# Kernel tuning notes

Measured on AMD Instinct MI355X. Metric: run time of the kernel, lower is better.

## Reference

```python
import jax, jax.numpy as jnp
import numpy as np

D_MODEL = 1024
N_HEADS = 16
HEAD_DIM = D_MODEL // N_HEADS
BATCH = 1
SEQLEN = 4096


def setup_inputs() -> dict:
    key = jax.random.key(0)
    k1, k2, k3 = jax.random.split(key, 3)
    x = jax.random.normal(k1, (BATCH, SEQLEN, D_MODEL), dtype=jnp.float32)
    # match typical Dense init scale so softmax isn't saturated
    Wqkv = jax.random.normal(k2, (D_MODEL, 3 * D_MODEL), dtype=jnp.float32) / np.sqrt(D_MODEL)
    Wout = jax.random.normal(k3, (D_MODEL, D_MODEL), dtype=jnp.float32) / np.sqrt(D_MODEL)
    return {"x": x, "Wqkv": Wqkv, "Wout": Wout}


def reference(x, Wqkv, Wout):
    b, l, d = x.shape
    qkv = x @ Wqkv  # [b, l, 3d]
    q, k, v = jnp.split(qkv, 3, axis=-1)
    # [b, l, d] -> [b, h, l, hd]
    def to_heads(t):
        return t.reshape(b, l, N_HEADS, HEAD_DIM).transpose(0, 2, 1, 3)
    q, k, v = to_heads(q), to_heads(k), to_heads(v)
    scale = 1.0 / np.sqrt(HEAD_DIM)
    attn = jnp.einsum('bhld,bhsd->bhls', q, k) * scale  # [b,h,l,l]
    causal_mask = jnp.tril(jnp.ones((l, l), dtype=bool))
    attn = jnp.where(causal_mask, attn, -jnp.inf)
    attn = jax.nn.softmax(attn, axis=-1)
    out = jnp.einsum('bhls,bhsd->bhld', attn, v)  # [b,h,l,hd]
    out = out.transpose(0, 2, 1, 3).reshape(b, l, d)
    return out @ Wout
```

## Files before the change

### kernel.cpp

```cpp
#include <hip/hip_runtime.h>

#define SEQ 4096
#define DM 1024
#define NH 16
#define HD 64

typedef __attribute__((ext_vector_type(8))) short short8;
typedef __attribute__((ext_vector_type(4))) short short4v;
typedef __attribute__((ext_vector_type(2))) short short2v;
typedef __attribute__((ext_vector_type(4))) float float4v;
typedef __attribute__((ext_vector_type(4))) int int4v;

__device__ __forceinline__ short f2bf(float f) {
    union { float f; unsigned u; } v; v.f = f;
    unsigned u = v.u;
    return (short)((u + 0x7fffu + ((u >> 16) & 1u)) >> 16);
}
__device__ __forceinline__ int cvtpk(float lo, float hi) {
    int r;
    asm("v_cvt_pk_bf16_f32 %0, %1, %2" : "=v"(r) : "v"(lo), "v"(hi));
    return r;
}

__device__ __forceinline__ void gload_lds16(const void* g, void* l) {
    __builtin_amdgcn_global_load_lds(
        (const __attribute__((address_space(1))) void*)g,
        (__attribute__((address_space(3))) void*)l, 16, 0, 0);
}

__global__ void cast_x(const float* __restrict__ in, short* __restrict__ out, int n4) {
    int i = blockIdx.x * blockDim.x + threadIdx.x;
    if (i < n4) {
        float4v x = ((const float4v*)in)[i];
        short4v o;
        o[0] = f2bf(x[0]); o[1] = f2bf(x[1]); o[2] = f2bf(x[2]); o[3] = f2bf(x[3]);
        ((short4v*)out)[i] = o;
    }
}

__global__ void transpose_cast(const float* __restrict__ in, short* __restrict__ out,
                               int H, int W, int scaled_rows, float scale) {
    __shared__ float tile[32][33];
    int bx = blockIdx.x * 32, by = blockIdx.y * 32;
    int tx = threadIdx.x, ty = threadIdx.y;
#pragma unroll
    for (int i = 0; i < 32; i += 8)
        tile[ty + i][tx] = in[(by + ty + i) * W + bx + tx];
    __syncthreads();
#pragma unroll
    for (int i = 0; i < 32; i += 8) {
        int orow = bx + ty + i;
        float sc = (orow < scaled_rows) ? scale : 1.0f;
        out[orow * H + by + tx] = f2bf(tile[tx][ty + i] * sc);
    }
}

__global__ void transpose_v(const short* __restrict__ qkv, short* __restrict__ vt) {
    __shared__ short tile[64][66];
    int h = blockIdx.z;
    int l0 = blockIdx.x * 64;
    int tx = threadIdx.x, ty = threadIdx.y;
#pragma unroll
    for (int i = 0; i < 8; i++) {
        int r = ty + i * 8;
        short2v v = *(const short2v*)&qkv[(l0 + r) * (3 * DM) + 2 * DM + h * HD + 2 * tx];
        tile[r][2 * tx] = v[0];
        tile[r][2 * tx + 1] = v[1];
    }
    __syncthreads();
#pragma unroll
    for (int i = 0; i < 8; i++) {
        int d = ty + i * 8;
        short2v v;
        v[0] = tile[2 * tx][d];
        v[1] = tile[2 * tx + 1][d];
        int s = l0 + 2 * tx;
        int soff = (s & ~31) | ((s & 12) << 1) | ((s & 16) >> 2) | (s & 3);
        *(short2v*)&vt[(h * HD + d) * SEQ + soff] = v;
    }
}

template <typename OutT>
__global__ __launch_bounds__(256) void gemm_bt(const short* __restrict__ A,
                                               const short* __restrict__ BT,
                                               OutT* __restrict__ C,
                                               int M, int N, int K) {
    __shared__ short As[128 * 32];
    __shared__ short Bs[128 * 32];
    int tid  = threadIdx.x;
    int m0   = blockIdx.y * 128;
    int n0   = blockIdx.x * 128;
    int w    = tid >> 6, lane = tid & 63;
    int wm   = w >> 1,  wn   = w & 1;
    int quad = lane >> 4, l15 = lane & 15;
    int srow = lane >> 2;
    int scol = (lane & 3) * 8;

    float4v acc[4][4];
#pragma unroll
    for (int mi = 0; mi < 4; mi++)
#pragma unroll
        for (int ni = 0; ni < 4; ni++)
            acc[mi][ni] = {0.f, 0.f, 0.f, 0.f};

    for (int k0 = 0; k0 < K; k0 += 32) {
        __syncthreads();
#pragma unroll
        for (int t = 0; t < 2; t++) {
            int chunk = w * 2 + t;
            int r = chunk * 16 + srow;
            gload_lds16(&A[(m0 + r) * K + k0 + scol], &As[chunk * 16 * 32]);
            gload_lds16(&BT[(n0 + r) * K + k0 + scol], &Bs[chunk * 16 * 32]);
        }
        __syncthreads();
        short8 a[4], b[4];
#pragma unroll
        for (int mi = 0; mi < 4; mi++)
            a[mi] = *(const short8*)&As[(wm * 64 + mi * 16 + l15) * 32 + quad * 8];
#pragma unroll
        for (int ni = 0; ni < 4; ni++)
            b[ni] = *(const short8*)&Bs[(wn * 64 + ni * 16 + l15) * 32 + quad * 8];
#pragma unroll
        for (int mi = 0; mi < 4; mi++)
#pragma unroll
            for (int ni = 0; ni < 4; ni++)
                acc[mi][ni] = __builtin_amdgcn_mfma_f32_16x16x32_bf16(a[mi], b[ni], acc[mi][ni], 0, 0, 0);
    }

#pragma unroll
    for (int mi = 0; mi < 4; mi++)
#pragma unroll
        for (int ni = 0; ni < 4; ni++)
#pragma unroll
            for (int r = 0; r < 4; r++) {
                int row = m0 + wm * 64 + mi * 16 + quad * 4 + r;
                int col = n0 + wn * 64 + ni * 16 + l15;
                float v = acc[mi][ni][r];
                if constexpr (sizeof(OutT) == 2) C[row * N + col] = (OutT)f2bf(v);
                else                             C[row * N + col] = (OutT)v;
            }
}

__global__ __launch_bounds__(256) void gemm_bt64(const short* __restrict__ A,
                                                 const short* __restrict__ BT,
                                                 float* __restrict__ C,
                                                 int M, int N, int K) {
    __shared__ short As[64 * 32];
    __shared__ short Bs[128 * 32];
    int tid  = threadIdx.x;
    int m0   = blockIdx.y * 64;
    int n0   = blockIdx.x * 128;
    int w    = tid >> 6, lane = tid & 63;
    int wm   = w >> 1,  wn   = w & 1;
    int quad = lane >> 4, l15 = lane & 15;
    int srow = lane >> 2;
    int scol = (lane & 3) * 8;

    float4v acc[2][4];
#pragma unroll
    for (int mi = 0; mi < 2; mi++)
#pragma unroll
        for (int ni = 0; ni < 4; ni++)
            acc[mi][ni] = {0.f, 0.f, 0.f, 0.f};

    for (int k0 = 0; k0 < K; k0 += 32) {
        __syncthreads();
        {
            int r = w * 16 + srow;
            gload_lds16(&A[(m0 + r) * K + k0 + scol], &As[w * 16 * 32]);
        }
#pragma unroll
        for (int t = 0; t < 2; t++) {
            int chunk = w * 2 + t;
            int r = chunk * 16 + srow;
            gload_lds16(&BT[(n0 + r) * K + k0 + scol], &Bs[chunk * 16 * 32]);
        }
        __syncthreads();
        short8 a[2], b[4];
#pragma unroll
        for (int mi = 0; mi < 2; mi++)
            a[mi] = *(const short8*)&As[(wm * 32 + mi * 16 + l15) * 32 + quad * 8];
#pragma unroll
        for (int ni = 0; ni < 4; ni++)
            b[ni] = *(const short8*)&Bs[(wn * 64 + ni * 16 + l15) * 32 + quad * 8];
#pragma unroll
        for (int mi = 0; mi < 2; mi++)
#pragma unroll
            for (int ni = 0; ni < 4; ni++)
                acc[mi][ni] = __builtin_amdgcn_mfma_f32_16x16x32_bf16(a[mi], b[ni], acc[mi][ni], 0, 0, 0);
    }

#pragma unroll
    for (int mi = 0; mi < 2; mi++)
#pragma unroll
        for (int ni = 0; ni < 4; ni++)
#pragma unroll
            for (int r = 0; r < 4; r++) {
                int row = m0 + wm * 32 + mi * 16 + quad * 4 + r;
                int col = n0 + wn * 64 + ni * 16 + l15;
                C[row * N + col] = acc[mi][ni][r];
            }
}

__global__ __launch_bounds__(256, 2) void attn_kernel(const short* __restrict__ qkv,
                                                      const short* __restrict__ vtp,
                                                      float* __restrict__ Of0,
                                                      float* __restrict__ Of1,
                                                      float* __restrict__ Of2,
                                                      float* __restrict__ Lf0,
                                                      float* __restrict__ Lf1,
                                                      float* __restrict__ Lf2) {
    __shared__ short Ks[3][64 * 64];
    __shared__ short Vs[3][64 * 64];
    int gid = blockIdx.x;
    int rr = gid & 7, qq = gid >> 3;
    int hb = qq / 48;
    int rem = qq - hb * 48;
    int h = rr + 8 * hb;
    int b = rem & 15;
    int j = rem >> 4;
    float* __restrict__ Of = (j == 0) ? Of0 : (j == 1) ? Of1 : Of2;
    float* __restrict__ Lf = (j == 0) ? Lf0 : (j == 1) ? Lf1 : Lf2;
    int B0 = 2 * b + 2;

    int tid = threadIdx.x;
    int w = tid >> 6, lane = tid & 63;
    int quad = lane >> 4, l15 = lane & 15;
    int rowb = w * 16;
    int lrow = lane >> 3;
    int cg   = (lane & 7) ^ lrow;
    int xr   = (l15 & 7) * 8;

    const short* Kg = qkv + DM + h * HD;
    const short* Vg = vtp + (h * HD) * SEQ;

    short8 onesv;
#pragma unroll
    for (int i = 0; i < 8; i++) onesv[i] = (short)0x3F80;

#pragma unroll 1
    for (int sg = 0; sg < 2; sg++) {
        int t, st0, stN;
        if (sg == 0) {
            t = b;
            st0 = 22 * j;
            stN = (22 * j + 22 < B0) ? 22 * j + 22 : B0;
        } else {
            t = 31 - b;
            int a0 = 22 * j - B0;
            st0 = (a0 > 0) ? a0 : 0;
            stN = 22 * j + 22 - B0;
        }
        if (st0 >= stN) continue;

        int q0 = t * 128;
        int qw = q0 + w * 32;

        short8 aq[2][2];
#pragma unroll
        for (int mi = 0; mi < 2; mi++)
#pragma unroll
            for (int kk = 0; kk < 2; kk++)
                aq[mi][kk] = *(const short8*)&qkv[(qw + mi * 16 + l15) * (3 * DM) + h * HD + kk * 32 + quad * 8];

        float4v lacc[2];
        float4v o[2][4];
#pragma unroll
        for (int mi = 0; mi < 2; mi++) {
            lacc[mi] = {0.f, 0.f, 0.f, 0.f};
#pragma unroll
            for (int dt = 0; dt < 4; dt++)
                o[mi][dt] = {0.f, 0.f, 0.f, 0.f};
        }

        auto stage = [&](int slot, int tt_) {
            int s0_ = tt_ * 64;
#pragma unroll
            for (int i = 0; i < 2; i++) {
                int r = rowb + i * 8;
                gload_lds16(&Kg[(s0_ + r + lrow) * (3 * DM) + cg * 8], &Ks[slot][r * 64]);
                gload_lds16(&Vg[(r + lrow) * SEQ + s0_ + cg * 8],      &Vs[slot][r * 64]);
            }
        };

        stage(0, st0);
        bool two = (st0 + 1 < stN);
        if (two) {
            stage(1, st0 + 1);
            asm volatile("s_waitcnt vmcnt(4)" ::: "memory");
        } else {
            asm volatile("s_waitcnt vmcnt(0)" ::: "memory");
        }
        __builtin_amdgcn_s_barrier();
        __builtin_amdgcn_sched_barrier(0);

        int sA = 0, sB = 1, sC = 2;
        for (int tt = st0; tt < stN; tt++) {
            int s0 = tt * 64;
            if (tt + 2 < stN) stage(sC, tt + 2);

            const short* Kb = &Ks[sA][0];
            const short* Vb = &Vs[sA][0];

            short8 kc[8], vc[8];
#pragma unroll
            for (int ni = 0; ni < 4; ni++)
#pragma unroll
                for (int kk = 0; kk < 2; kk++)
                    kc[ni * 2 + kk] = *(const short8*)&Kb[(ni * 16 + l15) * 64 + (((kk * 4 + quad) * 8) ^ xr)];
#pragma unroll
            for (int dt = 0; dt < 4; dt++)
#pragma unroll
                for (int pr = 0; pr < 2; pr++)
                    vc[dt * 2 + pr] = *(const short8*)&Vb[(dt * 16 + l15) * 64 + (((pr * 4 + quad) * 8) ^ xr)];

            float4v s[2][4];
            __builtin_amdgcn_s_setprio(1);
#pragma unroll
            for (int mi = 0; mi < 2; mi++)
#pragma unroll
                for (int ni = 0; ni < 4; ni++) {
                    float4v a = {0.f, 0.f, 0.f, 0.f};
#pragma unroll
                    for (int kk = 0; kk < 2; kk++)
                        a = __builtin_amdgcn_mfma_f32_16x16x32_bf16(kc[ni * 2 + kk], aq[mi][kk], a, 0, 0, 0);
                    s[mi][ni] = a;
                }
            __builtin_amdgcn_s_setprio(0);

            bool diag = (s0 + 63 > qw);
            if (diag) {
#pragma unroll
                for (int mi = 0; mi < 2; mi++) {
                    int qrow = qw + mi * 16 + l15;
#pragma unroll
                    for (int ni = 0; ni < 4; ni++)
#pragma unroll
                        for (int r = 0; r < 4; r++) {
                            float p = __builtin_amdgcn_exp2f(s[mi][ni][r]);
                            int scol = s0 + ni * 16 + quad * 4 + r;
                            s[mi][ni][r] = (scol <= qrow) ? p : 0.f;
                        }
                }
            } else {
#pragma unroll
                for (int mi = 0; mi < 2; mi++)
#pragma unroll
                    for (int ni = 0; ni < 4; ni++)
#pragma unroll
                        for (int r = 0; r < 4; r++)
                            s[mi][ni][r] = __builtin_amdgcn_exp2f(s[mi][ni][r]);
            }
            short8 pa[2][2];
#pragma unroll
            for (int mi = 0; mi < 2; mi++)
#pragma unroll
                for (int pr = 0; pr < 2; pr++) {
                    int4v wpk;
                    wpk[0] = cvtpk(s[mi][2 * pr][0], s[mi][2 * pr][1]);
                    wpk[1] = cvtpk(s[mi][2 * pr][2], s[mi][2 * pr][3]);
                    wpk[2] = cvtpk(s[mi][2 * pr + 1][0], s[mi][2 * pr + 1][1]);
                    wpk[3] = cvtpk(s[mi][2 * pr + 1][2], s[mi][2 * pr + 1][3]);
                    pa[mi][pr] = *(short8*)&wpk;
                }

            __builtin_amdgcn_s_setprio(1);
#pragma unroll
            for (int mi = 0; mi < 2; mi++)
#pragma unroll
                for (int pr = 0; pr < 2; pr++)
                    lacc[mi] = __builtin_amdgcn_mfma_f32_16x16x32_bf16(pa[mi][pr], onesv, lacc[mi], 0, 0, 0);
#pragma unroll
            for (int mi = 0; mi < 2; mi++)
#pragma unroll
                for (int dt = 0; dt < 4; dt++)
#pragma unroll
                    for (int pr = 0; pr < 2; pr++)
                        o[mi][dt] = __builtin_amdgcn_mfma_f32_16x16x32_bf16(pa[mi][pr], vc[dt * 2 + pr], o[mi][dt], 0, 0, 0);
            __builtin_amdgcn_s_setprio(0);

            asm volatile("s_waitcnt lgkmcnt(0)" ::: "memory");
            if (tt + 2 < stN) asm volatile("s_waitcnt vmcnt(4)" ::: "memory");
            else              asm volatile("s_waitcnt vmcnt(0)" ::: "memory");
            __builtin_amdgcn_s_barrier();
            __builtin_amdgcn_sched_barrier(0);
            int tmp = sA; sA = sB; sB = sC; sC = tmp;
        }

#pragma unroll
        for (int mi = 0; mi < 2; mi++)
#pragma unroll
            for (int r = 0; r < 4; r++) {
                int row = qw + mi * 16 + quad * 4 + r;
#pragma unroll
                for (int dt = 0; dt < 4; dt++)
                    Of[row * DM + h * HD + dt * 16 + l15] = o[mi][dt][r];
            }
        if (l15 == 0) {
#pragma unroll
            for (int mi = 0; mi < 2; mi++)
#pragma unroll
                for (int r = 0; r < 4; r++)
                    Lf[h * SEQ + qw + mi * 16 + quad * 4 + r] = lacc[mi][r];
        }
    }
}

__global__ void attn_finalize(const float* __restrict__ Of0, const float* __restrict__ Of1,
                              const float* __restrict__ Of2,
                              const float* __restrict__ Lf0, const float* __restrict__ Lf1,
                              const float* __restrict__ Lf2,
                              short* __restrict__ ao) {
    int i = blockIdx.x * blockDim.x + threadIdx.x;
    int q  = i >> 8;
    int c4 = i & 255;
    int h  = c4 >> 4;
    int t  = q >> 7;
    bool lowq = (t < 16);
    int b = lowq ? t : 31 - t;
    bool use0 = lowq || (b <= 9);
    bool use1 = (!lowq) || (b >= 11);
    bool use2 = !lowq;

    float l = 0.f;
    float4v acc = {0.f, 0.f, 0.f, 0.f};
    if (use0) {
        l += Lf0[h * SEQ + q];
        float4v a = ((const float4v*)Of0)[i];
        acc[0] += a[0]; acc[1] += a[1]; acc[2] += a[2]; acc[3] += a[3];
    }
    if (use1) {
        l += Lf1[h * SEQ + q];
        float4v a = ((const float4v*)Of1)[i];
        acc[0] += a[0]; acc[1] += a[1]; acc[2] += a[2]; acc[3] += a[3];
    }
    if (use2) {
        l += Lf2[h * SEQ + q];
        float4v a = ((const float4v*)Of2)[i];
        acc[0] += a[0]; acc[1] += a[1]; acc[2] += a[2]; acc[3] += a[3];
    }
    float inv = 1.0f / l;
    short4v o;
    o[0] = f2bf(acc[0] * inv);
    o[1] = f2bf(acc[1] * inv);
    o[2] = f2bf(acc[2] * inv);
    o[3] = f2bf(acc[3] * inv);
    ((short4v*)ao)[i] = o;
}

extern "C" void kernel_launch(void* const* d_in, const int* in_sizes, int n_in,
                              void* d_out, int out_size, void* d_ws, size_t ws_size,
                              hipStream_t stream) {
    const float* x    = (const float*)d_in[0];
    const float* Wqkv = (const float*)d_in[1];
    const float* Wout = (const float*)d_in[2];
    float* out = (float*)d_out;

    char* ws = (char*)d_ws;
    short* xb    = (short*)(ws);
    short* wqkvT = (short*)(ws + 8388608);
    float* Of0   = (float*)(ws);
    float* Of1   = (float*)(d_out);
    short* qkv   = (short*)(ws + 16777216);
    short* vt    = (short*)(ws + 41943040);
    short* ao    = (short*)(ws + 50331648);
    float* Of2   = (float*)(ws + 58720256);
    float* Lf0   = (float*)(ws + 75497472);
    float* Lf1   = (float*)(ws + 75759616);
    float* Lf2   = (float*)(ws + 76021760);
    short* woutT = (short*)(ws + 76283904);

    const float SC = 0.18033688011112042f;

    cast_x<<<4096, 256, 0, stream>>>(x, xb, (SEQ * DM) / 4);
    transpose_cast<<<dim3(3 * DM / 32, DM / 32), dim3(32, 8), 0, stream>>>(Wqkv, wqkvT, DM, 3 * DM, DM, SC);
    transpose_cast<<<dim3(DM / 32, DM / 32), dim3(32, 8), 0, stream>>>(Wout, woutT, DM, DM, 0, 1.0f);

    gemm_bt<short><<<dim3(3 * DM / 128, SEQ / 128), 256, 0, stream>>>(xb, wqkvT, qkv, SEQ, 3 * DM, DM);

    transpose_v<<<dim3(SEQ / 64, 1, NH), dim3(32, 8), 0, stream>>>(qkv, vt);

    attn_kernel<<<768, 256, 0, stream>>>(qkv, vt, Of0, Of1, Of2, Lf0, Lf1, Lf2);
    attn_finalize<<<(SEQ * DM / 4) / 256, 256, 0, stream>>>(Of0, Of1, Of2, Lf0, Lf1, Lf2, ao);

    gemm_bt64<<<dim3(DM / 128, SEQ / 64), 256, 0, stream>>>(ao, woutT, out, SEQ, DM, DM);
}
```

Before: 209.4 us.

## Software-pipeline PV MFMAs one tile behind QK and softmax in attention loop

The P·V and row-sum MFMAs for each KV tile are deferred to the next iteration, where they run right after the next tile's K fragments are read from LDS. Exp and packing of the current scores can then overlap with matrix work from the previous tile. The previous tile's P and V fragments are carried in registers (pa_p, vc_p), and a final epilogue drains the last tile after the loop. The ring-buffer slot rotation is simplified to a single modulo index. The carried fragments raise register pressure, which may hurt occupancy or cause spills.

```diff
diff --git a/kernel.cpp b/kernel.cpp
--- a/kernel.cpp
+++ b/kernel.cpp
@@ -294,25 +294,47 @@
         __builtin_amdgcn_s_barrier();
         __builtin_amdgcn_sched_barrier(0);
 
-        int sA = 0, sB = 1, sC = 2;
+        short8 pa_p[2][2];
+        short8 vc_p[8];
+        int si = 0;
         for (int tt = st0; tt < stN; tt++) {
             int s0 = tt * 64;
-            if (tt + 2 < stN) stage(sC, tt + 2);
-
-            const short* Kb = &Ks[sA][0];
-            const short* Vb = &Vs[sA][0];
-
-            short8 kc[8], vc[8];
+            int s2 = si + 2; if (s2 >= 3) s2 -= 3;
+            bool haveStage = (tt + 2 < stN);
+            if (haveStage) stage(s2, tt + 2);
+
+            const short* Kb = &Ks[si][0];
+            const short* Vb = &Vs[si][0];
+
+            short8 kc[8];
 #pragma unroll
             for (int ni = 0; ni < 4; ni++)
 #pragma unroll
                 for (int kk = 0; kk < 2; kk++)
                     kc[ni * 2 + kk] = *(const short8*)&Kb[(ni * 16 + l15) * 64 + (((kk * 4 + quad) * 8) ^ xr)];
+
+            if (tt > st0) {
+                __builtin_amdgcn_s_setprio(1);
+#pragma unroll
+                for (int mi = 0; mi < 2; mi++)
+#pragma unroll
+                    for (int pr = 0; pr < 2; pr++)
+                        lacc[mi] = __builtin_amdgcn_mfma_f32_16x16x32_bf16(pa_p[mi][pr], onesv, lacc[mi], 0, 0, 0);
+#pragma unroll
+                for (int mi = 0; mi < 2; mi++)
+#pragma unroll
+                    for (int dt = 0; dt < 4; dt++)
+#pragma unroll
+                        for (int pr = 0; pr < 2; pr++)
+                            o[mi][dt] = __builtin_amdgcn_mfma_f32_16x16x32_bf16(pa_p[mi][pr], vc_p[dt * 2 + pr], o[mi][dt], 0, 0, 0);
+                __builtin_amdgcn_s_setprio(0);
+            }
+
 #pragma unroll
             for (int dt = 0; dt < 4; dt++)
 #pragma unroll
                 for (int pr = 0; pr < 2; pr++)
-                    vc[dt * 2 + pr] = *(const short8*)&Vb[(dt * 16 + l15) * 64 + (((pr * 4 + quad) * 8) ^ xr)];
+                    vc_p[dt * 2 + pr] = *(const short8*)&Vb[(dt * 16 + l15) * 64 + (((pr * 4 + quad) * 8) ^ xr)];
 
             float4v s[2][4];
             __builtin_amdgcn_s_setprio(1);
@@ -351,7 +373,6 @@
                         for (int r = 0; r < 4; r++)
                             s[mi][ni][r] = __builtin_amdgcn_exp2f(s[mi][ni][r]);
             }
-            short8 pa[2][2];
 #pragma unroll
             for (int mi = 0; mi < 2; mi++)
 #pragma unroll
@@ -361,31 +382,31 @@
                     wpk[1] = cvtpk(s[mi][2 * pr][2], s[mi][2 * pr][3]);
                     wpk[2] = cvtpk(s[mi][2 * pr + 1][0], s[mi][2 * pr + 1][1]);
                     wpk[3] = cvtpk(s[mi][2 * pr + 1][2], s[mi][2 * pr + 1][3]);
-                    pa[mi][pr] = *(short8*)&wpk;
+                    pa_p[mi][pr] = *(short8*)&wpk;
                 }
 
-            __builtin_amdgcn_s_setprio(1);
-#pragma unroll
-            for (int mi = 0; mi < 2; mi++)
-#pragma unroll
-                for (int pr = 0; pr < 2; pr++)
-                    lacc[mi] = __builtin_amdgcn_mfma_f32_16x16x32_bf16(pa[mi][pr], onesv, lacc[mi], 0, 0, 0);
-#pragma unroll
-            for (int mi = 0; mi < 2; mi++)
-#pragma unroll
-                for (int dt = 0; dt < 4; dt++)
-#pragma unroll
-                    for (int pr = 0; pr < 2; pr++)
-                        o[mi][dt] = __builtin_amdgcn_mfma_f32_16x16x32_bf16(pa[mi][pr], vc[dt * 2 + pr], o[mi][dt], 0, 0, 0);
-            __builtin_amdgcn_s_setprio(0);
-
             asm volatile("s_waitcnt lgkmcnt(0)" ::: "memory");
-            if (tt + 2 < stN) asm volatile("s_waitcnt vmcnt(4)" ::: "memory");
-            else              asm volatile("s_waitcnt vmcnt(0)" ::: "memory");
+            if (haveStage) asm volatile("s_waitcnt vmcnt(4)" ::: "memory");
+            else           asm volatile("s_waitcnt vmcnt(0)" ::: "memory");
             __builtin_amdgcn_s_barrier();
             __builtin_amdgcn_sched_barrier(0);
-            int tmp = sA; sA = sB; sB = sC; sC = tmp;
-        }
+            si = si + 1; if (si >= 3) si = 0;
+        }
+
+        __builtin_amdgcn_s_setprio(1);
+#pragma unroll
+        for (int mi = 0; mi < 2; mi++)
+#pragma unroll
+            for (int pr = 0; pr < 2; pr++)
+                lacc[mi] = __builtin_amdgcn_mfma_f32_16x16x32_bf16(pa_p[mi][pr], onesv, lacc[mi], 0, 0, 0);
+#pragma unroll
+        for (int mi = 0; mi < 2; mi++)
+#pragma unroll
+            for (int dt = 0; dt < 4; dt++)
+#pragma unroll
+                for (int pr = 0; pr < 2; pr++)
+                    o[mi][dt] = __builtin_amdgcn_mfma_f32_16x16x32_bf16(pa_p[mi][pr], vc_p[dt * 2 + pr], o[mi][dt], 0, 0, 0);
+        __builtin_amdgcn_s_setprio(0);
 
 #pragma unroll
         for (int mi = 0; mi < 2; mi++)
```

Result: faster. 204.0 us (-2.6%).
